# Kernel optimization log

Measured on AMD Instinct MI355X. Metric: run time of the kernel, lower is better.

## Reference

```python
import math
import jax, jax.numpy as jnp
import numpy as np

HEADS = 8
D = 128            # model_dim
PE = D // 2        # position_embedding_size (query_positional_score=True)
MAXP = 32          # max_position_embeddings
LN_EPS = 1e-5


def setup_inputs() -> dict:
    key = jax.random.key(0)
    ks = jax.random.split(key, 7)
    bs, h, w = 8, 32, 32
    hidden_state = jax.random.normal(ks[0], (bs, h, w, D), dtype=jnp.float32)
    row_emb = jax.random.normal(ks[1], (2 * MAXP - 1, PE), dtype=jnp.float32) * 0.02
    col_emb = jax.random.normal(ks[2], (2 * MAXP - 1, PE), dtype=jnp.float32) * 0.02
    # torch Linear weights are (out_features, in_features)
    Wq = jax.random.normal(ks[3], (HEADS * D, D), dtype=jnp.float32) / math.sqrt(D)
    Wk = jax.random.normal(ks[4], (HEADS * D, D), dtype=jnp.float32) / math.sqrt(D)
    Wv = jax.random.normal(ks[5], (D, HEADS * D), dtype=jnp.float32) / math.sqrt(HEADS * D)
    bv = jnp.zeros((D,), dtype=jnp.float32)
    ln_g = jnp.ones((D,), dtype=jnp.float32)
    ln_b = jnp.zeros((D,), dtype=jnp.float32)
    return {"hidden_state": hidden_state, "row_emb": row_emb, "col_emb": col_emb,
            "Wq": Wq, "Wk": Wk, "Wv": Wv, "bv": bv, "ln_g": ln_g, "ln_b": ln_b}


def _layer_norm(x, g, b):
    mu = jnp.mean(x, axis=-1, keepdims=True)
    var = jnp.var(x, axis=-1, keepdims=True)
    return (x - mu) * jax.lax.rsqrt(var + LN_EPS) * g + b


def _forward(hidden_state, row_emb, col_emb, Wq, Wk, Wv, bv, ln_g, ln_b):
    bs, h, w, _ = hidden_state.shape
    x = _layer_norm(hidden_state, ln_g, ln_b)  # pre_norm=True
    sqrt_norm = math.sqrt(D)

    # relative indices (static, h == w == 32 here)
    deltas = np.arange(MAXP)[None, :] - np.arange(MAXP)[:, None]
    rel = deltas + MAXP - 1
    row_embeds = row_emb[rel[:w, :w]]  # (w, w, PE)
    col_embeds = col_emb[rel[:h, :h]]  # (h, h, PE)

    # projections; original does .view(bs, w, h, heads, D) on a (bs,h,w,heads*D) tensor
    q = jnp.einsum('bhwc,oc->bhwo', x, Wq).reshape(bs, w, h, HEADS, D)
    k = jnp.einsum('bhwc,oc->bhwo', x, Wk).reshape(bs, w, h, HEADS, D)

    q_row = q[..., :PE]
    q_col = q[..., PE:]
    row_scores = jnp.einsum('bijhd,ikd->bijhk', q_row, row_embeds)
    col_scores = jnp.einsum('bijhd,jld->bijhl', q_col, col_embeds)
    scores = (row_scores[..., :, None] + col_scores[..., None, :]) / sqrt_norm  # bijhkl
    scores = scores.transpose(0, 2, 1, 3, 5, 4)

    content = jnp.einsum('bijhd,bklhd->bijhkl', q, k) / sqrt_norm
    scores = scores + content.transpose(0, 2, 1, 3, 5, 4)  # (bs, h, w, heads, h, w)

    attn_shape = scores.shape
    probs = jax.nn.softmax(scores.reshape(*attn_shape[:-2], -1), axis=-1).reshape(attn_shape)

    # dropout omitted (inference / p=0)
    context = jnp.einsum('bijhkl,bkld->bijhd', probs, x)
    context = context.reshape(bs, h, w, HEADS * D)
    output = jnp.einsum('bhwc,oc->bhwo', context, Wv) + bv + x
    return output, probs


def reference(hidden_state, row_emb, col_emb, Wq, Wk, Wv, bv, ln_g, ln_b):
    return _forward(hidden_state, row_emb, col_emb, Wq, Wk, Wv, bv, ln_g, ln_b)
```

## Files before the change

### kernel.cpp

```cpp
#include <hip/hip_runtime.h>
#include <hip/hip_bf16.h>

#define HEADS 8
#define D 128
#define INV_SQRT_D 0.08838834764831845f

typedef unsigned short u16;
typedef unsigned int u32;
typedef __attribute__((ext_vector_type(8))) short short8;
typedef __attribute__((ext_vector_type(4))) float f32x4;

static __device__ inline float sbf2f(short s) {
    return __uint_as_float(((u32)(unsigned short)s) << 16);
}
static __device__ inline u16 f2bf(float f) {
    u32 u = __float_as_uint(f);
    return (u16)((u + 0x7FFFu + ((u >> 16) & 1u)) >> 16);
}
static __device__ inline float bf2f(u32 u) {
    return __uint_as_float(u << 16);
}
static __device__ inline u32 pk2bf(float a, float b) {
    return (u32)f2bf(a) | ((u32)f2bf(b) << 16);
}
static __device__ inline f32x4 mfma16(short8 a, short8 b, f32x4 c) {
    return __builtin_amdgcn_mfma_f32_16x16x32_bf16(a, b, c, 0, 0, 0);
}

__global__ __launch_bounds__(256) void k_wcvt(const float* __restrict__ Wq,
    const float* __restrict__ Wk, const float* __restrict__ Wv,
    u16* __restrict__ wqk, u16* __restrict__ wv)
{
    int idx = (blockIdx.x * 256 + threadIdx.x) * 4;
    const float* src;
    u16* dst;
    if (idx < 131072)      { src = Wq + idx;           dst = wqk + idx; }
    else if (idx < 262144) { src = Wk + (idx - 131072); dst = wqk + idx; }
    else                   { src = Wv + (idx - 262144); dst = wv + (idx - 262144); }
    f32x4 v = *(const f32x4*)src;
    u32 p0 = pk2bf(v[0], v[1]);
    u32 p1 = pk2bf(v[2], v[3]);
    *(uint2*)dst = make_uint2(p0, p1);
}

__global__ __launch_bounds__(256) void k_ln(const float* __restrict__ hs,
    const float* __restrict__ g, const float* __restrict__ b,
    float* __restrict__ xf, u16* __restrict__ xbf)
{
    int row  = blockIdx.x * 4 + (threadIdx.x >> 6);
    int lane = threadIdx.x & 63;
    const float* p = hs + (size_t)row * D + lane * 2;
    float2 v = *(const float2*)p;
    float s  = v.x + v.y;
    float s2 = v.x * v.x + v.y * v.y;
    #pragma unroll
    for (int off = 1; off < 64; off <<= 1) {
        s  += __shfl_xor(s, off);
        s2 += __shfl_xor(s2, off);
    }
    float mu  = s * 0.0078125f;
    float var = s2 * 0.0078125f - mu * mu;
    float inv = rsqrtf(var + 1e-5f);
    float2 o;
    o.x = (v.x - mu) * inv * g[lane * 2 + 0] + b[lane * 2 + 0];
    o.y = (v.y - mu) * inv * g[lane * 2 + 1] + b[lane * 2 + 1];
    *(float2*)(xf + (size_t)row * D + lane * 2) = o;
    *(u32*)(xbf + (size_t)row * D + lane * 2) = pk2bf(o.x, o.y);
}

__global__ __launch_bounds__(256) void k_xt(const float* __restrict__ xf,
    u16* __restrict__ xt)
{
    __shared__ __align__(16) u16 tl[128][136];
    int b = blockIdx.x, ch = blockIdx.y;
    int tid = threadIdx.x;
    const float* src = xf + ((size_t)b * 1024 + ch * 128) * 128;
    #pragma unroll
    for (int it = 0; it < 16; ++it) {
        int s = tid + it * 256;
        int p = s >> 5, d4 = (s & 31) * 4;
        f32x4 v = *(const f32x4*)(src + (size_t)p * 128 + d4);
        tl[d4 + 0][p] = f2bf(v[0]);
        tl[d4 + 1][p] = f2bf(v[1]);
        tl[d4 + 2][p] = f2bf(v[2]);
        tl[d4 + 3][p] = f2bf(v[3]);
    }
    __syncthreads();
    u16* dst = xt + (size_t)b * 131072 + ch * 128;
    #pragma unroll
    for (int i = 0; i < 8; ++i) {
        int d = (tid >> 4) + i * 16, c8 = (tid & 15) * 8;
        *(uint4*)(dst + (size_t)d * 1024 + c8) = *(const uint4*)&tl[d][c8];
    }
}

__global__ __launch_bounds__(256) void k_proj(const u16* __restrict__ xbf,
    const u16* __restrict__ wqk,
    u16* __restrict__ q_bf, u16* __restrict__ kt_bf)
{
    int tid = threadIdx.x;
    int w = tid >> 6, l = tid & 63, h = l >> 4, ln = l & 15;
    int t0 = blockIdx.x * 64 + w * 16;
    int o0 = blockIdx.y * 64;
    short8 a[4];
    #pragma unroll
    for (int s = 0; s < 4; ++s)
        a[s] = *(const short8*)(xbf + (size_t)(t0 + ln) * 128 + s * 32 + h * 8);
    f32x4 acc[4];
    #pragma unroll
    for (int n = 0; n < 4; ++n) acc[n] = f32x4{0.f, 0.f, 0.f, 0.f};
    #pragma unroll
    for (int n = 0; n < 4; ++n) {
        const u16* wsrc = wqk + (size_t)(o0 + n * 16 + ln) * 128;
        #pragma unroll
        for (int s = 0; s < 4; ++s) {
            short8 bf = *(const short8*)(wsrc + s * 32 + h * 8);
            acc[n] = mfma16(a[s], bf, acc[n]);
        }
    }
    bool isq = (o0 < 1024);
    int head = (o0 & 1023) >> 7;
    int od_base = (o0 & 127);
    u16* basep = isq ? q_bf : kt_bf;
    #pragma unroll
    for (int n = 0; n < 4; ++n) {
        int d0 = od_base + n * 16 + ln;
        #pragma unroll
        for (int r = 0; r < 4; ++r) {
            int t = t0 + h * 4 + r;
            int b = t >> 10, pos = t & 1023;
            size_t row;
            if (isq) row = (size_t)(b * 8 + head) * 1024 + pos;
            else { int I = pos >> 5, J = pos & 31; row = (size_t)(b * 8 + head) * 1024 + (J * 32 + I); }
            basep[row * 128 + d0] = f2bf(acc[n][r]);
        }
    }
}

__global__ __launch_bounds__(256, 2) void k_attn(const u16* __restrict__ q_bf,
    const u16* __restrict__ kt_bf, const u16* __restrict__ xt_bf,
    const float* __restrict__ row_emb, const float* __restrict__ col_emb,
    float* __restrict__ probs, u16* __restrict__ ctx_bf)
{
    __shared__ __align__(16) char P区[65536];
    __shared__ __align__(16) float rb_s[32 * 36];
    __shared__ __align__(16) float cb_s[32 * 64];
    __shared__ float wred[2][128];
    char* P = P区;
    u16* re_bf = (u16*)P区;
    u16* ce_bf = (u16*)(P区 + 4096);

    int tid = threadIdx.x;
    int w = tid >> 6, l = tid & 63, h = l >> 4, ln = l & 15;
    int qt = blockIdx.x, bh = blockIdx.y;
    int b = bh >> 3, head = bh & 7;
    int q0 = qt * 32;
    int I = qt;

    {
        int K = tid >> 3, d8 = (tid & 7) * 8;
        const float* src = row_emb + (size_t)(K - I + 31) * 64 + d8;
        f32x4 v0 = *(const f32x4*)src;
        f32x4 v1 = *(const f32x4*)(src + 4);
        *(uint4*)(re_bf + K * 64 + d8) = make_uint4(
            pk2bf(v0[0], v0[1]), pk2bf(v0[2], v0[3]),
            pk2bf(v1[0], v1[1]), pk2bf(v1[2], v1[3]));
    }
    #pragma unroll
    for (int it = 0; it < 2; ++it) {
        int s = tid + it * 256;
        int p = s >> 3, d8 = (s & 7) * 8;
        uint4 o;
        if (p < 63) {
            const float* src = col_emb + (size_t)p * 64 + d8;
            f32x4 v0 = *(const f32x4*)src;
            f32x4 v1 = *(const f32x4*)(src + 4);
            o = make_uint4(pk2bf(v0[0], v0[1]), pk2bf(v0[2], v0[3]),
                           pk2bf(v1[0], v1[1]), pk2bf(v1[2], v1[3]));
        } else o = make_uint4(0, 0, 0, 0);
        *(uint4*)(ce_bf + p * 64 + d8) = o;
    }

    short8 qa[2][4];
    const u16* qbase = q_bf + ((size_t)bh * 1024 + q0) * 128;
    #pragma unroll
    for (int m = 0; m < 2; ++m)
        #pragma unroll
        for (int s = 0; s < 4; ++s)
            qa[m][s] = *(const short8*)(qbase + (size_t)(m * 16 + ln) * 128 + s * 32 + h * 8);

    __syncthreads();

    if (w < 2) {
        int mt = w;
        f32x4 arb[2] = {f32x4{0,0,0,0}, f32x4{0,0,0,0}};
        #pragma unroll
        for (int s = 0; s < 2; ++s) {
            #pragma unroll
            for (int nt = 0; nt < 2; ++nt) {
                short8 bf = *(const short8*)(re_bf + (nt * 16 + ln) * 64 + s * 32 + h * 8);
                arb[nt] = mfma16(qa[mt][s], bf, arb[nt]);
            }
        }
        #pragma unroll
        for (int nt = 0; nt < 2; ++nt)
            #pragma unroll
            for (int r = 0; r < 4; ++r)
                rb_s[(mt * 16 + h * 4 + r) * 36 + nt * 16 + ln] = arb[nt][r];
    } else {
        int mt = w - 2;
        f32x4 acb[4] = {f32x4{0,0,0,0}, f32x4{0,0,0,0}, f32x4{0,0,0,0}, f32x4{0,0,0,0}};
        #pragma unroll
        for (int s = 0; s < 2; ++s) {
            #pragma unroll
            for (int nt = 0; nt < 4; ++nt) {
                short8 bf = *(const short8*)(ce_bf + (nt * 16 + ln) * 64 + s * 32 + h * 8);
                acb[nt] = mfma16(qa[mt][2 + s], bf, acb[nt]);
            }
        }
        #pragma unroll
        for (int nt = 0; nt < 4; ++nt)
            #pragma unroll
            for (int r = 0; r < 4; ++r)
                cb_s[(mt * 16 + h * 4 + r) * 64 + nt * 16 + ln] = acb[nt][r];
    }

    f32x4 acc[2][16];
    #pragma unroll
    for (int n = 0; n < 2; ++n)
        #pragma unroll
        for (int t = 0; t < 16; ++t) acc[n][t] = f32x4{0.f, 0.f, 0.f, 0.f};
    int kk0 = w * 256;
    const u16* kbase = kt_bf + ((size_t)bh * 1024 + kk0) * 128;
    #pragma unroll
    for (int t = 0; t < 16; ++t) {
        #pragma unroll
        for (int s = 0; s < 4; ++s) {
            short8 kf = *(const short8*)(kbase + (size_t)(t * 16 + ln) * 128 + s * 32 + h * 8);
            acc[0][t] = mfma16(kf, qa[0][s], acc[0][t]);
            acc[1][t] = mfma16(kf, qa[1][s], acc[1][t]);
        }
    }
    __syncthreads();

    f32x4 rbr[2][2];
    float cbr[2][8];
    #pragma unroll
    for (int n = 0; n < 2; ++n) {
        int J = n * 16 + ln;
        #pragma unroll
        for (int par = 0; par < 2; ++par)
            rbr[n][par] = *(const f32x4*)&rb_s[J * 36 + par * 16 + h * 4];
        #pragma unroll
        for (int lL = 0; lL < 8; ++lL) {
            int L = (kk0 >> 5) + lL;
            cbr[n][lL] = cb_s[J * 64 + (L - J + 31)];
        }
    }

    #pragma unroll
    for (int n = 0; n < 2; ++n) {
        float mx = -1e30f;
        #pragma unroll
        for (int t = 0; t < 16; ++t) {
            float cbv = cbr[n][t >> 1];
            #pragma unroll
            for (int r = 0; r < 4; ++r) {
                float v = (acc[n][t][r] + rbr[n][t & 1][r] + cbv) * INV_SQRT_D;
                acc[n][t][r] = v;
                mx = fmaxf(mx, v);
            }
        }
        mx = fmaxf(mx, __shfl_xor(mx, 16));
        mx = fmaxf(mx, __shfl_xor(mx, 32));
        if (l < 16) wred[0][w * 32 + n * 16 + ln] = mx;
    }
    __syncthreads();

    #pragma unroll
    for (int n = 0; n < 2; ++n) {
        int J = n * 16 + ln;
        float M = fmaxf(fmaxf(wred[0][J], wred[0][32 + J]),
                        fmaxf(wred[0][64 + J], wred[0][96 + J]));
        float sum = 0.f;
        #pragma unroll
        for (int t = 0; t < 16; ++t) {
            float p0 = __expf(acc[n][t][0] - M);
            float p1 = __expf(acc[n][t][1] - M);
            float p2 = __expf(acc[n][t][2] - M);
            float p3 = __expf(acc[n][t][3] - M);
            sum += (p0 + p1) + (p2 + p3);
            int kk = kk0 + t * 16 + h * 4;
            int byteoff = J * 2048 + ((kk * 2) ^ ((J & 7) << 4));
            *(uint2*)(P + byteoff) = make_uint2(pk2bf(p0, p1), pk2bf(p2, p3));
        }
        sum += __shfl_xor(sum, 16);
        sum += __shfl_xor(sum, 32);
        if (l < 16) wred[1][w * 32 + J] = sum;
    }
    __syncthreads();

    f32x4 cacc[2][2];
    #pragma unroll
    for (int m = 0; m < 2; ++m)
        #pragma unroll
        for (int n = 0; n < 2; ++n) cacc[m][n] = f32x4{0.f, 0.f, 0.f, 0.f};
    int d0 = w * 32;
    const u16* xb = xt_bf + (size_t)b * 131072;
    #pragma unroll 4
    for (int ks = 0; ks < 32; ++ks) {
        short8 pa[2];
        #pragma unroll
        for (int m = 0; m < 2; ++m) {
            int J = m * 16 + ln;
            int byteoff = J * 2048 + (((ks * 32 + h * 8) * 2) ^ ((J & 7) << 4));
            pa[m] = *(const short8*)(P + byteoff);
        }
        #pragma unroll
        for (int n = 0; n < 2; ++n) {
            short8 xf8 = *(const short8*)(xb + (size_t)(d0 + n * 16 + ln) * 1024 + ks * 32 + h * 8);
            cacc[0][n] = mfma16(pa[0], xf8, cacc[0][n]);
            cacc[1][n] = mfma16(pa[1], xf8, cacc[1][n]);
        }
    }
    #pragma unroll
    for (int m = 0; m < 2; ++m) {
        #pragma unroll
        for (int r = 0; r < 4; ++r) {
            int J = m * 16 + h * 4 + r;
            float lsum = wred[1][J] + wred[1][32 + J] + wred[1][64 + J] + wred[1][96 + J];
            float inv = 1.0f / lsum;
            u16* dst = ctx_bf + ((size_t)(b * 32 + J) * 32 + qt) * 1024 + head * 128 + d0;
            dst[ln]      = f2bf(cacc[m][0][r] * inv);
            dst[16 + ln] = f2bf(cacc[m][1][r] * inv);
        }
    }
    {
        int J = tid >> 3;
        float lsum = wred[1][J] + wred[1][32 + J] + wred[1][64 + J] + wred[1][96 + J];
        float inv = 1.0f / lsum;
        float* prow = probs + ((((size_t)(b * 32 + J) * 32 + qt) * 8 + head) << 10);
        #pragma unroll
        for (int i = 0; i < 16; ++i) {
            int kk = i * 64 + (tid & 7) * 8;
            int byteoff = J * 2048 + ((kk * 2) ^ ((J & 7) << 4));
            short8 pv = *(const short8*)(P + byteoff);
            float4 o0, o1;
            o0.x = sbf2f(pv[0]) * inv; o0.y = sbf2f(pv[1]) * inv;
            o0.z = sbf2f(pv[2]) * inv; o0.w = sbf2f(pv[3]) * inv;
            o1.x = sbf2f(pv[4]) * inv; o1.y = sbf2f(pv[5]) * inv;
            o1.z = sbf2f(pv[6]) * inv; o1.w = sbf2f(pv[7]) * inv;
            *(float4*)(prow + kk)     = o0;
            *(float4*)(prow + kk + 4) = o1;
        }
    }
}

__global__ __launch_bounds__(256) void k_out(const u16* __restrict__ ctx_bf,
    const u16* __restrict__ wv_bf, const float* __restrict__ bv,
    const float* __restrict__ xf, float* __restrict__ out)
{
    int tid = threadIdx.x;
    int w = tid >> 6, l = tid & 63, h = l >> 4, ln = l & 15;
    int wm = w >> 1, wn = w & 1;
    int t0 = blockIdx.x * 32 + wm * 16;
    int o0 = blockIdx.y * 64 + wn * 32;
    f32x4 acc[2] = {f32x4{0,0,0,0}, f32x4{0,0,0,0}};
    for (int ks = 0; ks < 32; ++ks) {
        short8 a = *(const short8*)(ctx_bf + (size_t)(t0 + ln) * 1024 + ks * 32 + h * 8);
        #pragma unroll
        for (int nt = 0; nt < 2; ++nt) {
            short8 bb = *(const short8*)(wv_bf + (size_t)(o0 + nt * 16 + ln) * 1024 + ks * 32 + h * 8);
            acc[nt] = mfma16(a, bb, acc[nt]);
        }
    }
    #pragma unroll
    for (int nt = 0; nt < 2; ++nt) {
        int o = o0 + nt * 16 + ln;
        float bvv = bv[o];
        #pragma unroll
        for (int r = 0; r < 4; ++r) {
            int t = t0 + h * 4 + r;
            out[(size_t)t * 128 + o] = acc[nt][r] + bvv + xf[(size_t)t * 128 + o];
        }
    }
}

extern "C" void kernel_launch(void* const* d_in, const int* in_sizes, int n_in,
                              void* d_out, int out_size, void* d_ws, size_t ws_size,
                              hipStream_t stream) {
    (void)in_sizes; (void)n_in; (void)out_size; (void)ws_size;
    const float* hs      = (const float*)d_in[0];
    const float* row_emb = (const float*)d_in[1];
    const float* col_emb = (const float*)d_in[2];
    const float* Wq      = (const float*)d_in[3];
    const float* Wk      = (const float*)d_in[4];
    const float* Wv      = (const float*)d_in[5];
    const float* bv      = (const float*)d_in[6];
    const float* ln_g    = (const float*)d_in[7];
    const float* ln_b    = (const float*)d_in[8];

    float* out   = (float*)d_out;
    float* probs = out + 1048576;

    char* ws = (char*)d_ws;
    float* xf     = (float*)(ws);
    u16*   xbf    = (u16*)(ws + 4194304);
    u16*   q_bf   = (u16*)(ws + 6291456);
    u16*   kt_bf  = (u16*)(ws + 23068672);
    u16*   xt     = (u16*)(ws + 39845888);
    u16*   wqk_bf = (u16*)(ws + 41943040);
    u16*   wv_bf  = (u16*)(ws + 42467328);
    u16*   ctx    = (u16*)(ws + 42729472);

    k_wcvt <<<384, 256, 0, stream>>>(Wq, Wk, Wv, wqk_bf, wv_bf);
    k_ln   <<<2048, 256, 0, stream>>>(hs, ln_g, ln_b, xf, xbf);
    k_xt   <<<dim3(8, 8), 256, 0, stream>>>(xf, xt);
    k_proj <<<dim3(128, 32), 256, 0, stream>>>(xbf, wqk_bf, q_bf, kt_bf);
    k_attn <<<dim3(32, 64), 256, 0, stream>>>(q_bf, kt_bf, xt, row_emb, col_emb, probs, ctx);
    k_out  <<<dim3(256, 2), 256, 0, stream>>>(ctx, wv_bf, bv, xf, out);
}
```

Before: 281.8 us.

## Halve attention query tile to 16 rows and fold softmax scale into Q

The attention kernel now handles 16 query rows per block instead of 32 and launches twice as many blocks. This halves shared memory and accumulator registers per block, which should allow more blocks per CU. The cost is that K and x are reloaded twice as often. Separately, Q is pre-scaled by log2(e)/sqrt(D) in the projection, so the softmax uses exp2f and skips the per-element multiply. The row and column positional biases now come from the pre-scaled Q, which changes bf16 rounding slightly.

```diff
diff --git a/kernel.cpp b/kernel.cpp
--- a/kernel.cpp
+++ b/kernel.cpp
@@ -3,7 +3,7 @@
 
 #define HEADS 8
 #define D 128
-#define INV_SQRT_D 0.08838834764831845f
+#define QSCALE 0.12751743f
 
 typedef unsigned short u16;
 typedef unsigned int u32;
@@ -16,9 +16,6 @@
 static __device__ inline u16 f2bf(float f) {
     u32 u = __float_as_uint(f);
     return (u16)((u + 0x7FFFu + ((u >> 16) & 1u)) >> 16);
-}
-static __device__ inline float bf2f(u32 u) {
-    return __uint_as_float(u << 16);
 }
 static __device__ inline u32 pk2bf(float a, float b) {
     return (u32)f2bf(a) | ((u32)f2bf(b) << 16);
@@ -119,6 +116,7 @@
         }
     }
     bool isq = (o0 < 1024);
+    float oscale = isq ? QSCALE : 1.0f;
     int head = (o0 & 1023) >> 7;
     int od_base = (o0 & 127);
     u16* basep = isq ? q_bf : kt_bf;
@@ -132,7 +130,7 @@
             size_t row;
             if (isq) row = (size_t)(b * 8 + head) * 1024 + pos;
             else { int I = pos >> 5, J = pos & 31; row = (size_t)(b * 8 + head) * 1024 + (J * 32 + I); }
-            basep[row * 128 + d0] = f2bf(acc[n][r]);
+            basep[row * 128 + d0] = f2bf(acc[n][r] * oscale);
         }
     }
 }
@@ -142,20 +140,20 @@
     const float* __restrict__ row_emb, const float* __restrict__ col_emb,
     float* __restrict__ probs, u16* __restrict__ ctx_bf)
 {
-    __shared__ __align__(16) char P区[65536];
-    __shared__ __align__(16) float rb_s[32 * 36];
-    __shared__ __align__(16) float cb_s[32 * 64];
-    __shared__ float wred[2][128];
-    char* P = P区;
-    u16* re_bf = (u16*)P区;
-    u16* ce_bf = (u16*)(P区 + 4096);
+    __shared__ __align__(16) char Praw[32768];
+    __shared__ __align__(16) float rb_s[16 * 36];
+    __shared__ __align__(16) float cb_s[16 * 64];
+    __shared__ float wred[2][64];
+    char* P = Praw;
+    u16* re_bf = (u16*)Praw;
+    u16* ce_bf = (u16*)(Praw + 4096);
 
     int tid = threadIdx.x;
     int w = tid >> 6, l = tid & 63, h = l >> 4, ln = l & 15;
-    int qt = blockIdx.x, bh = blockIdx.y;
+    int bx = blockIdx.x, bh = blockIdx.y;
     int b = bh >> 3, head = bh & 7;
-    int q0 = qt * 32;
-    int I = qt;
+    int I = bx >> 1;
+    int Jbase = (bx & 1) * 16;
 
     {
         int K = tid >> 3, d8 = (tid & 7) * 8;
@@ -181,55 +179,48 @@
         *(uint4*)(ce_bf + p * 64 + d8) = o;
     }
 
-    short8 qa[2][4];
-    const u16* qbase = q_bf + ((size_t)bh * 1024 + q0) * 128;
-    #pragma unroll
-    for (int m = 0; m < 2; ++m)
-        #pragma unroll
-        for (int s = 0; s < 4; ++s)
-            qa[m][s] = *(const short8*)(qbase + (size_t)(m * 16 + ln) * 128 + s * 32 + h * 8);
-
-    __syncthreads();
-
-    if (w < 2) {
-        int mt = w;
+    short8 qa[4];
+    const u16* qbase = q_bf + ((size_t)bh * 1024 + I * 32 + Jbase) * 128;
+    #pragma unroll
+    for (int s = 0; s < 4; ++s)
+        qa[s] = *(const short8*)(qbase + (size_t)ln * 128 + s * 32 + h * 8);
+
+    __syncthreads();
+
+    if (w == 0) {
         f32x4 arb[2] = {f32x4{0,0,0,0}, f32x4{0,0,0,0}};
         #pragma unroll
-        for (int s = 0; s < 2; ++s) {
+        for (int s = 0; s < 2; ++s)
             #pragma unroll
             for (int nt = 0; nt < 2; ++nt) {
                 short8 bf = *(const short8*)(re_bf + (nt * 16 + ln) * 64 + s * 32 + h * 8);
-                arb[nt] = mfma16(qa[mt][s], bf, arb[nt]);
+                arb[nt] = mfma16(qa[s], bf, arb[nt]);
             }
-        }
         #pragma unroll
         for (int nt = 0; nt < 2; ++nt)
             #pragma unroll
             for (int r = 0; r < 4; ++r)
-                rb_s[(mt * 16 + h * 4 + r) * 36 + nt * 16 + ln] = arb[nt][r];
-    } else {
-        int mt = w - 2;
-        f32x4 acb[4] = {f32x4{0,0,0,0}, f32x4{0,0,0,0}, f32x4{0,0,0,0}, f32x4{0,0,0,0}};
-        #pragma unroll
-        for (int s = 0; s < 2; ++s) {
-            #pragma unroll
-            for (int nt = 0; nt < 4; ++nt) {
-                short8 bf = *(const short8*)(ce_bf + (nt * 16 + ln) * 64 + s * 32 + h * 8);
-                acb[nt] = mfma16(qa[mt][2 + s], bf, acb[nt]);
+                rb_s[(h * 4 + r) * 36 + nt * 16 + ln] = arb[nt][r];
+    } else if (w <= 2) {
+        int pb = (w - 1) * 32;
+        f32x4 acb[2] = {f32x4{0,0,0,0}, f32x4{0,0,0,0}};
+        #pragma unroll
+        for (int s = 0; s < 2; ++s)
+            #pragma unroll
+            for (int nt = 0; nt < 2; ++nt) {
+                short8 bf = *(const short8*)(ce_bf + (pb + nt * 16 + ln) * 64 + s * 32 + h * 8);
+                acb[nt] = mfma16(qa[2 + s], bf, acb[nt]);
             }
-        }
-        #pragma unroll
-        for (int nt = 0; nt < 4; ++nt)
+        #pragma unroll
+        for (int nt = 0; nt < 2; ++nt)
             #pragma unroll
             for (int r = 0; r < 4; ++r)
-                cb_s[(mt * 16 + h * 4 + r) * 64 + nt * 16 + ln] = acb[nt][r];
-    }
-
-    f32x4 acc[2][16];
-    #pragma unroll
-    for (int n = 0; n < 2; ++n)
-        #pragma unroll
-        for (int t = 0; t < 16; ++t) acc[n][t] = f32x4{0.f, 0.f, 0.f, 0.f};
+                cb_s[(h * 4 + r) * 64 + pb + nt * 16 + ln] = acb[nt][r];
+    }
+
+    f32x4 acc[16];
+    #pragma unroll
+    for (int t = 0; t < 16; ++t) acc[t] = f32x4{0.f, 0.f, 0.f, 0.f};
     int kk0 = w * 256;
     const u16* kbase = kt_bf + ((size_t)bh * 1024 + kk0) * 128;
     #pragma unroll
@@ -237,113 +228,94 @@
         #pragma unroll
         for (int s = 0; s < 4; ++s) {
             short8 kf = *(const short8*)(kbase + (size_t)(t * 16 + ln) * 128 + s * 32 + h * 8);
-            acc[0][t] = mfma16(kf, qa[0][s], acc[0][t]);
-            acc[1][t] = mfma16(kf, qa[1][s], acc[1][t]);
-        }
-    }
-    __syncthreads();
-
-    f32x4 rbr[2][2];
-    float cbr[2][8];
-    #pragma unroll
-    for (int n = 0; n < 2; ++n) {
-        int J = n * 16 + ln;
-        #pragma unroll
-        for (int par = 0; par < 2; ++par)
-            rbr[n][par] = *(const f32x4*)&rb_s[J * 36 + par * 16 + h * 4];
-        #pragma unroll
-        for (int lL = 0; lL < 8; ++lL) {
-            int L = (kk0 >> 5) + lL;
-            cbr[n][lL] = cb_s[J * 64 + (L - J + 31)];
-        }
-    }
-
-    #pragma unroll
-    for (int n = 0; n < 2; ++n) {
+            acc[t] = mfma16(kf, qa[s], acc[t]);
+        }
+    }
+    __syncthreads();
+
+    f32x4 rbr[2];
+    float cbr[8];
+    #pragma unroll
+    for (int par = 0; par < 2; ++par)
+        rbr[par] = *(const f32x4*)&rb_s[ln * 36 + par * 16 + h * 4];
+    #pragma unroll
+    for (int lL = 0; lL < 8; ++lL) {
+        int L = (kk0 >> 5) + lL;
+        cbr[lL] = cb_s[ln * 64 + (L - (Jbase + ln) + 31)];
+    }
+
+    {
         float mx = -1e30f;
         #pragma unroll
         for (int t = 0; t < 16; ++t) {
-            float cbv = cbr[n][t >> 1];
+            float cbv = cbr[t >> 1];
             #pragma unroll
             for (int r = 0; r < 4; ++r) {
-                float v = (acc[n][t][r] + rbr[n][t & 1][r] + cbv) * INV_SQRT_D;
-                acc[n][t][r] = v;
+                float v = acc[t][r] + rbr[t & 1][r] + cbv;
+                acc[t][r] = v;
                 mx = fmaxf(mx, v);
             }
         }
         mx = fmaxf(mx, __shfl_xor(mx, 16));
         mx = fmaxf(mx, __shfl_xor(mx, 32));
-        if (l < 16) wred[0][w * 32 + n * 16 + ln] = mx;
-    }
-    __syncthreads();
-
-    #pragma unroll
-    for (int n = 0; n < 2; ++n) {
-        int J = n * 16 + ln;
-        float M = fmaxf(fmaxf(wred[0][J], wred[0][32 + J]),
-                        fmaxf(wred[0][64 + J], wred[0][96 + J]));
+        if (l < 16) wred[0][w * 16 + ln] = mx;
+    }
+    __syncthreads();
+
+    {
+        float M = fmaxf(fmaxf(wred[0][ln], wred[0][16 + ln]),
+                        fmaxf(wred[0][32 + ln], wred[0][48 + ln]));
         float sum = 0.f;
         #pragma unroll
         for (int t = 0; t < 16; ++t) {
-            float p0 = __expf(acc[n][t][0] - M);
-            float p1 = __expf(acc[n][t][1] - M);
-            float p2 = __expf(acc[n][t][2] - M);
-            float p3 = __expf(acc[n][t][3] - M);
+            float p0 = exp2f(acc[t][0] - M);
+            float p1 = exp2f(acc[t][1] - M);
+            float p2 = exp2f(acc[t][2] - M);
+            float p3 = exp2f(acc[t][3] - M);
             sum += (p0 + p1) + (p2 + p3);
             int kk = kk0 + t * 16 + h * 4;
-            int byteoff = J * 2048 + ((kk * 2) ^ ((J & 7) << 4));
+            int byteoff = ln * 2048 + ((kk * 2) ^ ((ln & 7) << 4));
             *(uint2*)(P + byteoff) = make_uint2(pk2bf(p0, p1), pk2bf(p2, p3));
         }
         sum += __shfl_xor(sum, 16);
         sum += __shfl_xor(sum, 32);
-        if (l < 16) wred[1][w * 32 + J] = sum;
-    }
-    __syncthreads();
-
-    f32x4 cacc[2][2];
-    #pragma unroll
-    for (int m = 0; m < 2; ++m)
-        #pragma unroll
-        for (int n = 0; n < 2; ++n) cacc[m][n] = f32x4{0.f, 0.f, 0.f, 0.f};
+        if (l < 16) wred[1][w * 16 + ln] = sum;
+    }
+    __syncthreads();
+
+    f32x4 cacc[2] = {f32x4{0,0,0,0}, f32x4{0,0,0,0}};
     int d0 = w * 32;
     const u16* xb = xt_bf + (size_t)b * 131072;
     #pragma unroll 4
     for (int ks = 0; ks < 32; ++ks) {
-        short8 pa[2];
-        #pragma unroll
-        for (int m = 0; m < 2; ++m) {
-            int J = m * 16 + ln;
-            int byteoff = J * 2048 + (((ks * 32 + h * 8) * 2) ^ ((J & 7) << 4));
-            pa[m] = *(const short8*)(P + byteoff);
-        }
-        #pragma unroll
-        for (int n = 0; n < 2; ++n) {
-            short8 xf8 = *(const short8*)(xb + (size_t)(d0 + n * 16 + ln) * 1024 + ks * 32 + h * 8);
-            cacc[0][n] = mfma16(pa[0], xf8, cacc[0][n]);
-            cacc[1][n] = mfma16(pa[1], xf8, cacc[1][n]);
-        }
-    }
-    #pragma unroll
-    for (int m = 0; m < 2; ++m) {
-        #pragma unroll
-        for (int r = 0; r < 4; ++r) {
-            int J = m * 16 + h * 4 + r;
-            float lsum = wred[1][J] + wred[1][32 + J] + wred[1][64 + J] + wred[1][96 + J];
-            float inv = 1.0f / lsum;
-            u16* dst = ctx_bf + ((size_t)(b * 32 + J) * 32 + qt) * 1024 + head * 128 + d0;
-            dst[ln]      = f2bf(cacc[m][0][r] * inv);
-            dst[16 + ln] = f2bf(cacc[m][1][r] * inv);
-        }
+        int byteoff = ln * 2048 + (((ks * 32 + h * 8) * 2) ^ ((ln & 7) << 4));
+        short8 pa = *(const short8*)(P + byteoff);
+        #pragma unroll
+        for (int nt = 0; nt < 2; ++nt) {
+            short8 xf8 = *(const short8*)(xb + (size_t)(d0 + nt * 16 + ln) * 1024 + ks * 32 + h * 8);
+            cacc[nt] = mfma16(pa, xf8, cacc[nt]);
+        }
+    }
+    #pragma unroll
+    for (int r = 0; r < 4; ++r) {
+        int j = h * 4 + r;
+        int J = Jbase + j;
+        float lsum = wred[1][j] + wred[1][16 + j] + wred[1][32 + j] + wred[1][48 + j];
+        float inv = 1.0f / lsum;
+        u16* dst = ctx_bf + ((size_t)(b * 32 + J) * 32 + I) * 1024 + head * 128 + d0;
+        dst[ln]      = f2bf(cacc[0][r] * inv);
+        dst[16 + ln] = f2bf(cacc[1][r] * inv);
     }
     {
-        int J = tid >> 3;
-        float lsum = wred[1][J] + wred[1][32 + J] + wred[1][64 + J] + wred[1][96 + J];
+        int j = tid >> 4;
+        int J = Jbase + j;
+        float lsum = wred[1][j] + wred[1][16 + j] + wred[1][32 + j] + wred[1][48 + j];
         float inv = 1.0f / lsum;
-        float* prow = probs + ((((size_t)(b * 32 + J) * 32 + qt) * 8 + head) << 10);
-        #pragma unroll
-        for (int i = 0; i < 16; ++i) {
-            int kk = i * 64 + (tid & 7) * 8;
-            int byteoff = J * 2048 + ((kk * 2) ^ ((J & 7) << 4));
+        float* prow = probs + ((((size_t)(b * 32 + J) * 32 + I) * 8 + head) << 10);
+        #pragma unroll
+        for (int i = 0; i < 8; ++i) {
+            int kk = i * 128 + (tid & 15) * 8;
+            int byteoff = j * 2048 + ((kk * 2) ^ ((j & 7) << 4));
             short8 pv = *(const short8*)(P + byteoff);
             float4 o0, o1;
             o0.x = sbf2f(pv[0]) * inv; o0.y = sbf2f(pv[1]) * inv;
@@ -417,6 +389,6 @@
     k_ln   <<<2048, 256, 0, stream>>>(hs, ln_g, ln_b, xf, xbf);
     k_xt   <<<dim3(8, 8), 256, 0, stream>>>(xf, xt);
     k_proj <<<dim3(128, 32), 256, 0, stream>>>(xbf, wqk_bf, q_bf, kt_bf);
-    k_attn <<<dim3(32, 64), 256, 0, stream>>>(q_bf, kt_bf, xt, row_emb, col_emb, probs, ctx);
+    k_attn <<<dim3(64, 64), 256, 0, stream>>>(q_bf, kt_bf, xt, row_emb, col_emb, probs, ctx);
     k_out  <<<dim3(256, 2), 256, 0, stream>>>(ctx, wv_bf, bv, xf, out);
 }
```

After: 346.2 us. +22.9%, slower.

## Split positional bias into separate kernel and widen attention blocks to 512 threads

Applied to the files above, without the earlier changes.

Moves the row/column positional-bias MFMAs out of the attention kernel into a new k_bias kernel that writes precomputed biases to workspace. k_attn now runs 512 threads with 8 waves, each handling 128 keys, and uses a swizzled block order. Q is prescaled by log2(e)/sqrt(D) in the projection so softmax can use exp2 without a per-element multiply. Probabilities are written straight from registers instead of being re-read from bf16 shared memory. The costs are an extra kernel launch, extra global traffic for the bias tensors, and a changed rounding point for the scores.

```diff
diff --git a/kernel.cpp b/kernel.cpp
--- a/kernel.cpp
+++ b/kernel.cpp
@@ -3,28 +3,30 @@
 
 #define HEADS 8
 #define D 128
-#define INV_SQRT_D 0.08838834764831845f
+#define QSCALE 0.12751743f
 
 typedef unsigned short u16;
 typedef unsigned int u32;
 typedef __attribute__((ext_vector_type(8))) short short8;
 typedef __attribute__((ext_vector_type(4))) float f32x4;
 
-static __device__ inline float sbf2f(short s) {
-    return __uint_as_float(((u32)(unsigned short)s) << 16);
-}
 static __device__ inline u16 f2bf(float f) {
     u32 u = __float_as_uint(f);
     return (u16)((u + 0x7FFFu + ((u >> 16) & 1u)) >> 16);
 }
-static __device__ inline float bf2f(u32 u) {
-    return __uint_as_float(u << 16);
-}
 static __device__ inline u32 pk2bf(float a, float b) {
     return (u32)f2bf(a) | ((u32)f2bf(b) << 16);
 }
 static __device__ inline f32x4 mfma16(short8 a, short8 b, f32x4 c) {
     return __builtin_amdgcn_mfma_f32_16x16x32_bf16(a, b, c, 0, 0, 0);
+}
+static __device__ inline short8 cvt8(const float* e) {
+    f32x4 v0 = *(const f32x4*)e;
+    f32x4 v1 = *(const f32x4*)(e + 4);
+    union { uint4 u; short8 s; } x;
+    x.u = make_uint4(pk2bf(v0[0], v0[1]), pk2bf(v0[2], v0[3]),
+                     pk2bf(v1[0], v1[1]), pk2bf(v1[2], v1[3]));
+    return x.s;
 }
 
 __global__ __launch_bounds__(256) void k_wcvt(const float* __restrict__ Wq,
@@ -38,9 +40,7 @@
     else if (idx < 262144) { src = Wk + (idx - 131072); dst = wqk + idx; }
     else                   { src = Wv + (idx - 262144); dst = wv + (idx - 262144); }
     f32x4 v = *(const f32x4*)src;
-    u32 p0 = pk2bf(v[0], v[1]);
-    u32 p1 = pk2bf(v[2], v[3]);
-    *(uint2*)dst = make_uint2(p0, p1);
+    *(uint2*)dst = make_uint2(pk2bf(v[0], v[1]), pk2bf(v[2], v[3]));
 }
 
 __global__ __launch_bounds__(256) void k_ln(const float* __restrict__ hs,
@@ -119,6 +119,7 @@
         }
     }
     bool isq = (o0 < 1024);
+    float oscale = isq ? QSCALE : 1.0f;
     int head = (o0 & 1023) >> 7;
     int od_base = (o0 & 127);
     u16* basep = isq ? q_bf : kt_bf;
@@ -132,141 +133,123 @@
             size_t row;
             if (isq) row = (size_t)(b * 8 + head) * 1024 + pos;
             else { int I = pos >> 5, J = pos & 31; row = (size_t)(b * 8 + head) * 1024 + (J * 32 + I); }
-            basep[row * 128 + d0] = f2bf(acc[n][r]);
-        }
-    }
-}
-
-__global__ __launch_bounds__(256, 2) void k_attn(const u16* __restrict__ q_bf,
-    const u16* __restrict__ kt_bf, const u16* __restrict__ xt_bf,
+            basep[row * 128 + d0] = f2bf(acc[n][r] * oscale);
+        }
+    }
+}
+
+__global__ __launch_bounds__(256) void k_bias(const u16* __restrict__ q_bf,
     const float* __restrict__ row_emb, const float* __restrict__ col_emb,
-    float* __restrict__ probs, u16* __restrict__ ctx_bf)
-{
-    __shared__ __align__(16) char P区[65536];
-    __shared__ __align__(16) float rb_s[32 * 36];
-    __shared__ __align__(16) float cb_s[32 * 64];
-    __shared__ float wred[2][128];
-    char* P = P区;
-    u16* re_bf = (u16*)P区;
-    u16* ce_bf = (u16*)(P区 + 4096);
-
+    float* __restrict__ rbias, float* __restrict__ cbias)
+{
+    __shared__ __align__(16) float cbf[32][68];
     int tid = threadIdx.x;
     int w = tid >> 6, l = tid & 63, h = l >> 4, ln = l & 15;
-    int qt = blockIdx.x, bh = blockIdx.y;
-    int b = bh >> 3, head = bh & 7;
-    int q0 = qt * 32;
-    int I = qt;
-
-    {
-        int K = tid >> 3, d8 = (tid & 7) * 8;
-        const float* src = row_emb + (size_t)(K - I + 31) * 64 + d8;
-        f32x4 v0 = *(const f32x4*)src;
-        f32x4 v1 = *(const f32x4*)(src + 4);
-        *(uint4*)(re_bf + K * 64 + d8) = make_uint4(
-            pk2bf(v0[0], v0[1]), pk2bf(v0[2], v0[3]),
-            pk2bf(v1[0], v1[1]), pk2bf(v1[2], v1[3]));
-    }
-    #pragma unroll
-    for (int it = 0; it < 2; ++it) {
-        int s = tid + it * 256;
-        int p = s >> 3, d8 = (s & 7) * 8;
-        uint4 o;
-        if (p < 63) {
-            const float* src = col_emb + (size_t)p * 64 + d8;
-            f32x4 v0 = *(const f32x4*)src;
-            f32x4 v1 = *(const f32x4*)(src + 4);
-            o = make_uint4(pk2bf(v0[0], v0[1]), pk2bf(v0[2], v0[3]),
-                           pk2bf(v1[0], v1[1]), pk2bf(v1[2], v1[3]));
-        } else o = make_uint4(0, 0, 0, 0);
-        *(uint4*)(ce_bf + p * 64 + d8) = o;
-    }
-
-    short8 qa[2][4];
-    const u16* qbase = q_bf + ((size_t)bh * 1024 + q0) * 128;
-    #pragma unroll
-    for (int m = 0; m < 2; ++m)
-        #pragma unroll
-        for (int s = 0; s < 4; ++s)
-            qa[m][s] = *(const short8*)(qbase + (size_t)(m * 16 + ln) * 128 + s * 32 + h * 8);
-
-    __syncthreads();
-
+    int blk = blockIdx.x;
+    int bh = blk >> 5, I = blk & 31;
+    const u16* qb = q_bf + ((size_t)bh * 1024 + I * 32) * 128;
+    size_t obase = (size_t)blk * 1024;
     if (w < 2) {
-        int mt = w;
-        f32x4 arb[2] = {f32x4{0,0,0,0}, f32x4{0,0,0,0}};
-        #pragma unroll
-        for (int s = 0; s < 2; ++s) {
-            #pragma unroll
-            for (int nt = 0; nt < 2; ++nt) {
-                short8 bf = *(const short8*)(re_bf + (nt * 16 + ln) * 64 + s * 32 + h * 8);
-                arb[nt] = mfma16(qa[mt][s], bf, arb[nt]);
-            }
-        }
-        #pragma unroll
-        for (int nt = 0; nt < 2; ++nt)
+        short8 a0 = *(const short8*)(qb + (size_t)(w * 16 + ln) * 128 + h * 8);
+        short8 a1 = *(const short8*)(qb + (size_t)(w * 16 + ln) * 128 + 32 + h * 8);
+        f32x4 o[2] = {f32x4{0,0,0,0}, f32x4{0,0,0,0}};
+        #pragma unroll
+        for (int n = 0; n < 2; ++n) {
+            int K = n * 16 + ln;
+            const float* e = row_emb + (size_t)(K - I + 31) * 64 + h * 8;
+            o[n] = mfma16(a0, cvt8(e), o[n]);
+            o[n] = mfma16(a1, cvt8(e + 32), o[n]);
+        }
+        #pragma unroll
+        for (int n = 0; n < 2; ++n)
             #pragma unroll
             for (int r = 0; r < 4; ++r)
-                rb_s[(mt * 16 + h * 4 + r) * 36 + nt * 16 + ln] = arb[nt][r];
+                rbias[obase + (size_t)(w * 16 + h * 4 + r) * 32 + n * 16 + ln] = o[n][r];
     } else {
-        int mt = w - 2;
-        f32x4 acb[4] = {f32x4{0,0,0,0}, f32x4{0,0,0,0}, f32x4{0,0,0,0}, f32x4{0,0,0,0}};
-        #pragma unroll
-        for (int s = 0; s < 2; ++s) {
-            #pragma unroll
-            for (int nt = 0; nt < 4; ++nt) {
-                short8 bf = *(const short8*)(ce_bf + (nt * 16 + ln) * 64 + s * 32 + h * 8);
-                acb[nt] = mfma16(qa[mt][2 + s], bf, acb[nt]);
-            }
-        }
-        #pragma unroll
-        for (int nt = 0; nt < 4; ++nt)
+        int m = w - 2;
+        short8 a0 = *(const short8*)(qb + (size_t)(m * 16 + ln) * 128 + 64 + h * 8);
+        short8 a1 = *(const short8*)(qb + (size_t)(m * 16 + ln) * 128 + 96 + h * 8);
+        f32x4 o[4] = {f32x4{0,0,0,0}, f32x4{0,0,0,0}, f32x4{0,0,0,0}, f32x4{0,0,0,0}};
+        #pragma unroll
+        for (int n = 0; n < 4; ++n) {
+            int p = n * 16 + ln;
+            if (p > 62) p = 62;
+            const float* e = col_emb + (size_t)p * 64 + h * 8;
+            o[n] = mfma16(a0, cvt8(e), o[n]);
+            o[n] = mfma16(a1, cvt8(e + 32), o[n]);
+        }
+        #pragma unroll
+        for (int n = 0; n < 4; ++n)
             #pragma unroll
             for (int r = 0; r < 4; ++r)
-                cb_s[(mt * 16 + h * 4 + r) * 64 + nt * 16 + ln] = acb[nt][r];
-    }
-
-    f32x4 acc[2][16];
+                cbf[m * 16 + h * 4 + r][n * 16 + ln] = o[n][r];
+    }
+    __syncthreads();
+    int J = tid >> 3, L0 = (tid & 7) * 4;
+    float4 g;
+    g.x = cbf[J][L0 + 0 - J + 31];
+    g.y = cbf[J][L0 + 1 - J + 31];
+    g.z = cbf[J][L0 + 2 - J + 31];
+    g.w = cbf[J][L0 + 3 - J + 31];
+    *(float4*)(cbias + obase + (size_t)J * 32 + L0) = g;
+}
+
+__global__ __launch_bounds__(512, 4) void k_attn(const u16* __restrict__ q_bf,
+    const u16* __restrict__ kt_bf, const u16* __restrict__ xt_bf,
+    const float* __restrict__ rbias, const float* __restrict__ cbias,
+    float* __restrict__ probs, u16* __restrict__ ctx_bf)
+{
+    __shared__ __align__(16) char P[65536];
+    __shared__ float wred[2][256];
+    __shared__ float linv_s[32];
+
+    int tid = threadIdx.x;
+    int w = tid >> 6, l = tid & 63, h = l >> 4, ln = l & 15;
+    int flat = blockIdx.x;
+    int swz = (flat & 7) * 256 + (flat >> 3);
+    int bh = swz >> 5, I = swz & 31;
+    int b = bh >> 3, head = bh & 7;
+    int kk0 = w * 128;
+
+    f32x4 acc[2][8];
     #pragma unroll
     for (int n = 0; n < 2; ++n)
         #pragma unroll
-        for (int t = 0; t < 16; ++t) acc[n][t] = f32x4{0.f, 0.f, 0.f, 0.f};
-    int kk0 = w * 256;
+        for (int t = 0; t < 8; ++t) acc[n][t] = f32x4{0.f, 0.f, 0.f, 0.f};
     const u16* kbase = kt_bf + ((size_t)bh * 1024 + kk0) * 128;
-    #pragma unroll
-    for (int t = 0; t < 16; ++t) {
-        #pragma unroll
-        for (int s = 0; s < 4; ++s) {
+    const u16* qbase = q_bf + ((size_t)bh * 1024 + I * 32) * 128;
+    #pragma unroll
+    for (int s = 0; s < 4; ++s) {
+        short8 q0 = *(const short8*)(qbase + (size_t)ln * 128 + s * 32 + h * 8);
+        short8 q1 = *(const short8*)(qbase + (size_t)(16 + ln) * 128 + s * 32 + h * 8);
+        #pragma unroll
+        for (int t = 0; t < 8; ++t) {
             short8 kf = *(const short8*)(kbase + (size_t)(t * 16 + ln) * 128 + s * 32 + h * 8);
-            acc[0][t] = mfma16(kf, qa[0][s], acc[0][t]);
-            acc[1][t] = mfma16(kf, qa[1][s], acc[1][t]);
-        }
-    }
-    __syncthreads();
-
-    f32x4 rbr[2][2];
-    float cbr[2][8];
+            acc[0][t] = mfma16(kf, q0, acc[0][t]);
+            acc[1][t] = mfma16(kf, q1, acc[1][t]);
+        }
+    }
+
+    const float* rbase = rbias + (size_t)(bh * 32 + I) * 1024;
+    const float* cbase = cbias + (size_t)(bh * 32 + I) * 1024;
+    f32x4 rbr[2][2], cbr[2];
     #pragma unroll
     for (int n = 0; n < 2; ++n) {
         int J = n * 16 + ln;
-        #pragma unroll
-        for (int par = 0; par < 2; ++par)
-            rbr[n][par] = *(const f32x4*)&rb_s[J * 36 + par * 16 + h * 4];
-        #pragma unroll
-        for (int lL = 0; lL < 8; ++lL) {
-            int L = (kk0 >> 5) + lL;
-            cbr[n][lL] = cb_s[J * 64 + (L - J + 31)];
-        }
+        rbr[n][0] = *(const f32x4*)(rbase + J * 32 + h * 4);
+        rbr[n][1] = *(const f32x4*)(rbase + J * 32 + 16 + h * 4);
+        cbr[n]    = *(const f32x4*)(cbase + J * 32 + w * 4);
     }
 
     #pragma unroll
     for (int n = 0; n < 2; ++n) {
         float mx = -1e30f;
         #pragma unroll
-        for (int t = 0; t < 16; ++t) {
+        for (int t = 0; t < 8; ++t) {
             float cbv = cbr[n][t >> 1];
             #pragma unroll
             for (int r = 0; r < 4; ++r) {
-                float v = (acc[n][t][r] + rbr[n][t & 1][r] + cbv) * INV_SQRT_D;
+                float v = acc[n][t][r] + rbr[n][t & 1][r] + cbv;
                 acc[n][t][r] = v;
                 mx = fmaxf(mx, v);
             }
@@ -280,80 +263,71 @@
     #pragma unroll
     for (int n = 0; n < 2; ++n) {
         int J = n * 16 + ln;
-        float M = fmaxf(fmaxf(wred[0][J], wred[0][32 + J]),
-                        fmaxf(wred[0][64 + J], wred[0][96 + J]));
+        float M = wred[0][J];
+        #pragma unroll
+        for (int w2 = 1; w2 < 8; ++w2) M = fmaxf(M, wred[0][w2 * 32 + J]);
         float sum = 0.f;
         #pragma unroll
-        for (int t = 0; t < 16; ++t) {
-            float p0 = __expf(acc[n][t][0] - M);
-            float p1 = __expf(acc[n][t][1] - M);
-            float p2 = __expf(acc[n][t][2] - M);
-            float p3 = __expf(acc[n][t][3] - M);
+        for (int t = 0; t < 8; ++t) {
+            float p0 = exp2f(acc[n][t][0] - M);
+            float p1 = exp2f(acc[n][t][1] - M);
+            float p2 = exp2f(acc[n][t][2] - M);
+            float p3 = exp2f(acc[n][t][3] - M);
+            acc[n][t] = f32x4{p0, p1, p2, p3};
             sum += (p0 + p1) + (p2 + p3);
             int kk = kk0 + t * 16 + h * 4;
-            int byteoff = J * 2048 + ((kk * 2) ^ ((J & 7) << 4));
-            *(uint2*)(P + byteoff) = make_uint2(pk2bf(p0, p1), pk2bf(p2, p3));
+            *(uint2*)(P + J * 2048 + ((kk * 2) ^ ((J & 7) << 4))) =
+                make_uint2(pk2bf(p0, p1), pk2bf(p2, p3));
         }
         sum += __shfl_xor(sum, 16);
         sum += __shfl_xor(sum, 32);
         if (l < 16) wred[1][w * 32 + J] = sum;
     }
     __syncthreads();
-
-    f32x4 cacc[2][2];
-    #pragma unroll
-    for (int m = 0; m < 2; ++m)
-        #pragma unroll
-        for (int n = 0; n < 2; ++n) cacc[m][n] = f32x4{0.f, 0.f, 0.f, 0.f};
-    int d0 = w * 32;
-    const u16* xb = xt_bf + (size_t)b * 131072;
+    if (tid < 32) {
+        float s = 0.f;
+        #pragma unroll
+        for (int w2 = 0; w2 < 8; ++w2) s += wred[1][w2 * 32 + tid];
+        linv_s[tid] = 1.0f / s;
+    }
+    __syncthreads();
+
+    #pragma unroll
+    for (int n = 0; n < 2; ++n) {
+        int J = n * 16 + ln;
+        float inv = linv_s[J];
+        float* prow = probs + ((((size_t)(b * 32 + J) * 32 + I) * 8 + head) << 10)
+                    + kk0 + h * 4;
+        #pragma unroll
+        for (int t = 0; t < 8; ++t) {
+            *(float4*)(prow + t * 16) = make_float4(
+                acc[n][t][0] * inv, acc[n][t][1] * inv,
+                acc[n][t][2] * inv, acc[n][t][3] * inv);
+        }
+    }
+
+    f32x4 cacc[2] = {f32x4{0,0,0,0}, f32x4{0,0,0,0}};
+    int d0 = w * 16;
+    const u16* xb = xt_bf + (size_t)b * 131072 + (size_t)(d0 + ln) * 1024 + h * 8;
     #pragma unroll 4
     for (int ks = 0; ks < 32; ++ks) {
-        short8 pa[2];
+        short8 xf8 = *(const short8*)(xb + ks * 32);
         #pragma unroll
         for (int m = 0; m < 2; ++m) {
             int J = m * 16 + ln;
-            int byteoff = J * 2048 + (((ks * 32 + h * 8) * 2) ^ ((J & 7) << 4));
-            pa[m] = *(const short8*)(P + byteoff);
-        }
-        #pragma unroll
-        for (int n = 0; n < 2; ++n) {
-            short8 xf8 = *(const short8*)(xb + (size_t)(d0 + n * 16 + ln) * 1024 + ks * 32 + h * 8);
-            cacc[0][n] = mfma16(pa[0], xf8, cacc[0][n]);
-            cacc[1][n] = mfma16(pa[1], xf8, cacc[1][n]);
-        }
-    }
-    #pragma unroll
-    for (int m = 0; m < 2; ++m) {
+            short8 pa = *(const short8*)(P + J * 2048 +
+                (((ks * 32 + h * 8) * 2) ^ ((J & 7) << 4)));
+            cacc[m] = mfma16(pa, xf8, cacc[m]);
+        }
+    }
+    #pragma unroll
+    for (int m = 0; m < 2; ++m)
         #pragma unroll
         for (int r = 0; r < 4; ++r) {
             int J = m * 16 + h * 4 + r;
-            float lsum = wred[1][J] + wred[1][32 + J] + wred[1][64 + J] + wred[1][96 + J];
-            float inv = 1.0f / lsum;
-            u16* dst = ctx_bf + ((size_t)(b * 32 + J) * 32 + qt) * 1024 + head * 128 + d0;
-            dst[ln]      = f2bf(cacc[m][0][r] * inv);
-            dst[16 + ln] = f2bf(cacc[m][1][r] * inv);
-        }
-    }
-    {
-        int J = tid >> 3;
-        float lsum = wred[1][J] + wred[1][32 + J] + wred[1][64 + J] + wred[1][96 + J];
-        float inv = 1.0f / lsum;
-        float* prow = probs + ((((size_t)(b * 32 + J) * 32 + qt) * 8 + head) << 10);
-        #pragma unroll
-        for (int i = 0; i < 16; ++i) {
-            int kk = i * 64 + (tid & 7) * 8;
-            int byteoff = J * 2048 + ((kk * 2) ^ ((J & 7) << 4));
-            short8 pv = *(const short8*)(P + byteoff);
-            float4 o0, o1;
-            o0.x = sbf2f(pv[0]) * inv; o0.y = sbf2f(pv[1]) * inv;
-            o0.z = sbf2f(pv[2]) * inv; o0.w = sbf2f(pv[3]) * inv;
-            o1.x = sbf2f(pv[4]) * inv; o1.y = sbf2f(pv[5]) * inv;
-            o1.z = sbf2f(pv[6]) * inv; o1.w = sbf2f(pv[7]) * inv;
-            *(float4*)(prow + kk)     = o0;
-            *(float4*)(prow + kk + 4) = o1;
-        }
-    }
+            ctx_bf[((size_t)(b * 32 + J) * 32 + I) * 1024 + head * 128 + d0 + ln] =
+                f2bf(cacc[m][r] * linv_s[J]);
+        }
 }
 
 __global__ __launch_bounds__(256) void k_out(const u16* __restrict__ ctx_bf,
@@ -412,11 +386,14 @@
     u16*   wqk_bf = (u16*)(ws + 41943040);
     u16*   wv_bf  = (u16*)(ws + 42467328);
     u16*   ctx    = (u16*)(ws + 42729472);
+    float* rbias  = (float*)(ws + 59506688);
+    float* cbias  = (float*)(ws + 67895296);
 
     k_wcvt <<<384, 256, 0, stream>>>(Wq, Wk, Wv, wqk_bf, wv_bf);
     k_ln   <<<2048, 256, 0, stream>>>(hs, ln_g, ln_b, xf, xbf);
     k_xt   <<<dim3(8, 8), 256, 0, stream>>>(xf, xt);
     k_proj <<<dim3(128, 32), 256, 0, stream>>>(xbf, wqk_bf, q_bf, kt_bf);
-    k_attn <<<dim3(32, 64), 256, 0, stream>>>(q_bf, kt_bf, xt, row_emb, col_emb, probs, ctx);
+    k_bias <<<2048, 256, 0, stream>>>(q_bf, row_emb, col_emb, rbias, cbias);
+    k_attn <<<2048, 512, 0, stream>>>(q_bf, kt_bf, xt, rbias, cbias, probs, ctx);
     k_out  <<<dim3(256, 2), 256, 0, stream>>>(ctx, wv_bf, bv, xf, out);
 }
```

Result: no change. 276.5 us (-1.9%).
